# Kernel tuning notes

Measured on AMD Instinct MI355X. Metric: run time of the kernel, lower is better.

Reference implementation:

```python
import jax, jax.numpy as jnp
import numpy as np

N = 50000      # nodes
E = 800000     # edges
DIN = 500      # input feature dim
H = 128        # hidden dim
C = 40         # num classes
B = 10000      # batch_size (labeled nodes)
L = 9          # n_layers
K = 5          # topk neighbors
ALPHA = 0.5
THETA = 1.0
ETA = 0.5


def setup_inputs() -> dict:
    key = jax.random.key(0)
    ks = jax.random.split(key, 10)
    x = jax.random.normal(ks[0], (N, DIN), jnp.float32)
    edge_index = jax.random.randint(ks[1], (2, E), 0, N, dtype=jnp.int32)
    edge_weight = jax.random.uniform(ks[2], (E,), jnp.float32)
    y = jax.random.randint(ks[3], (B,), 0, C, dtype=jnp.int32)
    W1 = jax.random.normal(ks[4], (DIN, H), jnp.float32) * 0.05
    b1 = jnp.zeros((H,), jnp.float32)
    conv_w1 = jax.random.normal(ks[5], (L, H, H), jnp.float32) * 0.05
    conv_w2 = jax.random.normal(ks[6], (L, H, H), jnp.float32) * 0.05
    W2 = jax.random.normal(ks[7], (H, C), jnp.float32) * 0.05
    b2 = jnp.zeros((C,), jnp.float32)
    return dict(x=x, edge_index=edge_index, edge_weight=edge_weight, y=y,
                batch_size=B, W1=W1, b1=b1, conv_w1=conv_w1, conv_w2=conv_w2,
                W2=W2, b2=b2)


def _spmm(edge_index, edge_weight, h):
    # out[row] += w * h[col]  (sparse adj_t @ h)
    row, col = edge_index[0], edge_index[1]
    msg = h[col] * edge_weight[:, None]           # [E, H]
    return jax.ops.segment_sum(msg, row, num_segments=N)


def reference(x, edge_index, edge_weight, y, batch_size, W1, b1, conv_w1, conv_w2, W2, b2):
    # eval mode: dropout is identity, no diagonal mask in label fusion
    h = jax.nn.relu(x @ W1 + b1)                  # [N, H]
    x0 = h
    for l in range(L):
        beta = float(np.log(THETA / (l + 1) + 1.0))
        p = _spmm(edge_index, edge_weight, h) * (1.0 - ALPHA)   # propagated, scaled
        xr = ALPHA * x0                                          # initial residual
        out = ((1.0 - beta) * p + beta * (p @ conv_w1[l])
               + (1.0 - beta) * xr + beta * (xr @ conv_w2[l]))
        h = jax.nn.relu(h + out)
    emb = h[:batch_size]                          # [B, H]
    logits = h @ W2 + b2
    p_lc = jax.nn.log_softmax(logits[:batch_size], axis=1)       # [B, C]
    # kNN label fusion: cosine similarity, topk, exp-weighted one-hot sum
    an = emb / jnp.clip(jnp.linalg.norm(emb, axis=1, keepdims=True), 1e-8)
    sim = an @ an.T                               # [B, B]
    vals, idx = jax.lax.top_k(sim, K)             # [B, K]
    w = jnp.exp(jax.lax.stop_gradient(vals))      # topk computed under no_grad
    onehot = jax.nn.one_hot(y, C, dtype=jnp.float32)             # [B, C]
    fused = jnp.einsum('bk,bkc->bc', w, onehot[idx])             # [B, C]
    p_sim = jax.nn.log_softmax(fused, axis=1)
    final = ETA * p_lc + (1.0 - ETA) * p_sim
    return final, emb
```

## Files before the change

### kernel.cpp

```cpp
#include <hip/hip_runtime.h>
#include <hip/hip_bf16.h>
#include <math.h>

#define Nn  50000
#define NR  50048
#define En  800000
#define DIN 500
#define Hd  128
#define Cc  40
#define Bb  10000
#define Ll  9
#define KT  5

typedef short bf16x8 __attribute__((ext_vector_type(8)));
typedef unsigned short u16x8 __attribute__((ext_vector_type(8)));
typedef float f32x4 __attribute__((ext_vector_type(4)));

__device__ inline float bf2f(unsigned short u) {
  union { unsigned int i; float f; } c; c.i = (unsigned int)u << 16; return c.f;
}
__device__ inline unsigned short f2bf(float f) {
  __hip_bfloat16 b = __float2bfloat16(f);
  return *(unsigned short*)&b;
}

__global__ __launch_bounds__(256) void k_pack_w1(const float* __restrict__ W1,
                                                 unsigned short* __restrict__ W1p) {
  const int id = blockIdx.x * 256 + threadIdx.x;
  if (id >= 65536) return;
  const int j = id & 7, col = (id >> 3) & 127, qk = id >> 10;
  const int k = (qk >> 2) * 32 + (qk & 3) * 8 + j;
  W1p[id] = f2bf((k < DIN) ? W1[(size_t)k * Hd + col] : 0.f);
}

__global__ __launch_bounds__(256) void k_pack_wc(const float* __restrict__ cw1,
    const float* __restrict__ cw2, unsigned short* __restrict__ Wcp) {
  const int id = blockIdx.x * 256 + threadIdx.x;
  if (id >= 294912) return;
  const int j = id & 7, col = (id >> 3) & 127, qk = (id >> 10) & 31, l = id >> 15;
  const int k = (qk >> 2) * 32 + (qk & 3) * 8 + j;
  float v;
  if (k < 128) v = cw1[((size_t)l * 128 + k) * 128 + col];
  else         v = 0.5f * cw2[((size_t)l * 128 + (k - 128)) * 128 + col];
  Wcp[id] = f2bf(v);
}

__global__ __launch_bounds__(256) void k_in(const float* __restrict__ x,
    const unsigned short* __restrict__ W1p, const float* __restrict__ b1,
    unsigned short* __restrict__ hb, unsigned short* __restrict__ x0b) {
  const int tid = threadIdx.x;
  const int wv = tid >> 6, lane = tid & 63;
  const int lrow = lane & 15, quad = lane >> 4;
  const int row0 = blockIdx.x * 64;
  const int ar = row0 + wv * 16 + lrow;
  f32x4 acc[8];
#pragma unroll
  for (int t = 0; t < 8; ++t) acc[t] = (f32x4){0.f, 0.f, 0.f, 0.f};

  for (int kk = 0; kk < 16; ++kk) {
    const int kbase = kk * 32 + quad * 8;
    float av[8];
    if (ar < Nn) {
      if (kk < 15) {
        const float4 p0 = *(const float4*)(x + (size_t)ar * DIN + kbase);
        const float4 p1 = *(const float4*)(x + (size_t)ar * DIN + kbase + 4);
        av[0] = p0.x; av[1] = p0.y; av[2] = p0.z; av[3] = p0.w;
        av[4] = p1.x; av[5] = p1.y; av[6] = p1.z; av[7] = p1.w;
      } else {
#pragma unroll
        for (int j = 0; j < 8; ++j)
          av[j] = (kbase + j < DIN) ? x[(size_t)ar * DIN + kbase + j] : 0.f;
      }
    } else {
#pragma unroll
      for (int j = 0; j < 8; ++j) av[j] = 0.f;
    }
    bf16x8 af;
#pragma unroll
    for (int j = 0; j < 8; ++j) af[j] = (short)f2bf(av[j]);
#pragma unroll
    for (int nt = 0; nt < 8; ++nt) {
      const bf16x8 bf = *(const bf16x8*)(W1p + ((size_t)(kk * 4 + quad) * 128 + nt * 16 + lrow) * 8);
      acc[nt] = __builtin_amdgcn_mfma_f32_16x16x32_bf16(af, bf, acc[nt], 0, 0, 0);
    }
  }

  __shared__ float sacc[64 * 132];
#pragma unroll
  for (int nt = 0; nt < 8; ++nt)
#pragma unroll
    for (int i = 0; i < 4; ++i)
      sacc[(wv * 16 + quad * 4 + i) * 132 + nt * 16 + lrow] = acc[nt][i];
  __syncthreads();

  const int row = tid >> 2, cs = (tid & 3) * 32;
  const int gr = row0 + row;
  if (gr < Nn) {
#pragma unroll
    for (int g = 0; g < 4; ++g) {
      const int c0 = cs + g * 8;
      float v[8];
#pragma unroll
      for (int j = 0; j < 8; ++j)
        v[j] = fmaxf(sacc[row * 132 + c0 + j] + b1[c0 + j], 0.f);
      u16x8 ob;
#pragma unroll
      for (int j = 0; j < 8; ++j) ob[j] = f2bf(v[j]);
      *(u16x8*)(hb + (size_t)gr * Hd + c0) = ob;
      *(u16x8*)(x0b + (size_t)gr * Hd + c0) = ob;
    }
  }
}

__global__ void k_hist(const int* __restrict__ rows, int* __restrict__ counts) {
  int e = blockIdx.x * 256 + threadIdx.x;
  if (e < En) atomicAdd(&counts[rows[e]], 1);
}

__global__ __launch_bounds__(1024) void k_scan(const int* __restrict__ counts,
                                               int* __restrict__ ptr) {
  __shared__ int buf[1024];
  __shared__ int s_base;
  const int tid = threadIdx.x;
  if (tid == 0) { s_base = 0; ptr[0] = 0; }
  __syncthreads();
  for (int start = 0; start < Nn; start += 1024) {
    int i = start + tid;
    int v = (i < Nn) ? counts[i] : 0;
    buf[tid] = v;
    __syncthreads();
    for (int off = 1; off < 1024; off <<= 1) {
      int t = (tid >= off) ? buf[tid - off] : 0;
      __syncthreads();
      buf[tid] += t;
      __syncthreads();
    }
    if (i < Nn) ptr[i + 1] = s_base + buf[tid];
    __syncthreads();
    if (tid == 0) s_base += buf[1023];
    __syncthreads();
  }
}

__global__ void k_scatter(const int* __restrict__ rows, const int* __restrict__ cols,
                          const float* __restrict__ w, const int* __restrict__ ptr,
                          int* __restrict__ fill, int* __restrict__ csr_col,
                          float* __restrict__ csr_w) {
  int e = blockIdx.x * 256 + threadIdx.x;
  if (e >= En) return;
  int r = rows[e];
  int pos = atomicAdd(&fill[r], 1);
  int d = ptr[r] + pos;
  csr_col[d] = cols[e];
  csr_w[d] = w[e];
}

__global__ __launch_bounds__(256) void k_spmm(const int* __restrict__ ptr,
    const int* __restrict__ csr_col, const float* __restrict__ csr_w,
    const unsigned short* __restrict__ hb, unsigned short* __restrict__ pb) {
  const int wave = (blockIdx.x * 256 + threadIdx.x) >> 6;
  const int lane = threadIdx.x & 63;
  const int g = lane >> 4;
  const int fl = lane & 15;
  if (wave >= Nn) return;
  const int s = ptr[wave], e_end = ptr[wave + 1];
  float acc[8];
#pragma unroll
  for (int j = 0; j < 8; ++j) acc[j] = 0.f;

  auto acc8 = [&](uint4 v, float w) {
    union { unsigned int i; float f; } t;
    t.i = v.x << 16;         acc[0] += w * t.f;
    t.i = v.x & 0xFFFF0000u; acc[1] += w * t.f;
    t.i = v.y << 16;         acc[2] += w * t.f;
    t.i = v.y & 0xFFFF0000u; acc[3] += w * t.f;
    t.i = v.z << 16;         acc[4] += w * t.f;
    t.i = v.z & 0xFFFF0000u; acc[5] += w * t.f;
    t.i = v.w << 16;         acc[6] += w * t.f;
    t.i = v.w & 0xFFFF0000u; acc[7] += w * t.f;
  };

  int e = s + g;
  for (; e + 12 < e_end; e += 16) {
    const int c0 = csr_col[e];
    const int c1 = csr_col[e + 4];
    const int c2 = csr_col[e + 8];
    const int c3 = csr_col[e + 12];
    const float w0 = csr_w[e];
    const float w1 = csr_w[e + 4];
    const float w2 = csr_w[e + 8];
    const float w3 = csr_w[e + 12];
    const uint4 v0 = *(const uint4*)(hb + (size_t)c0 * Hd + fl * 8);
    const uint4 v1 = *(const uint4*)(hb + (size_t)c1 * Hd + fl * 8);
    const uint4 v2 = *(const uint4*)(hb + (size_t)c2 * Hd + fl * 8);
    const uint4 v3 = *(const uint4*)(hb + (size_t)c3 * Hd + fl * 8);
    acc8(v0, w0); acc8(v1, w1); acc8(v2, w2); acc8(v3, w3);
  }
  for (; e + 4 < e_end; e += 8) {
    const int c0 = csr_col[e];
    const int c1 = csr_col[e + 4];
    const float w0 = csr_w[e];
    const float w1 = csr_w[e + 4];
    const uint4 v0 = *(const uint4*)(hb + (size_t)c0 * Hd + fl * 8);
    const uint4 v1 = *(const uint4*)(hb + (size_t)c1 * Hd + fl * 8);
    acc8(v0, w0); acc8(v1, w1);
  }
  if (e < e_end) {
    const int c = csr_col[e];
    const float w = csr_w[e];
    const uint4 v = *(const uint4*)(hb + (size_t)c * Hd + fl * 8);
    acc8(v, w);
  }
#pragma unroll
  for (int j = 0; j < 8; ++j) acc[j] += __shfl_xor(acc[j], 16);
#pragma unroll
  for (int j = 0; j < 8; ++j) acc[j] += __shfl_xor(acc[j], 32);
  if (g == 0) {
    uint4 o;
    o.x = (unsigned int)f2bf(0.5f * acc[0]) | ((unsigned int)f2bf(0.5f * acc[1]) << 16);
    o.y = (unsigned int)f2bf(0.5f * acc[2]) | ((unsigned int)f2bf(0.5f * acc[3]) << 16);
    o.z = (unsigned int)f2bf(0.5f * acc[4]) | ((unsigned int)f2bf(0.5f * acc[5]) << 16);
    o.w = (unsigned int)f2bf(0.5f * acc[6]) | ((unsigned int)f2bf(0.5f * acc[7]) << 16);
    *(uint4*)(pb + (size_t)wave * Hd + fl * 8) = o;
  }
}

__global__ __launch_bounds__(256) void k_layer(const unsigned short* __restrict__ pb,
    const unsigned short* __restrict__ x0b, const unsigned short* __restrict__ Wcp,
    unsigned short* __restrict__ hb, float beta) {
  const int tid = threadIdx.x;
  const int wv = tid >> 6, lane = tid & 63;
  const int lrow = lane & 15, quad = lane >> 4;
  const int row0 = blockIdx.x * 64;
  const int ar = row0 + wv * 16 + lrow;
  f32x4 acc[8];
#pragma unroll
  for (int t = 0; t < 8; ++t) acc[t] = (f32x4){0.f, 0.f, 0.f, 0.f};

#pragma unroll
  for (int kk = 0; kk < 8; ++kk) {
    const unsigned short* src = (kk < 4) ? pb : x0b;
    const int ko = (kk & 3) * 32 + quad * 8;
    const bf16x8 af = *(const bf16x8*)(src + (size_t)ar * Hd + ko);
#pragma unroll
    for (int nt = 0; nt < 8; ++nt) {
      const bf16x8 bf = *(const bf16x8*)(Wcp + ((size_t)(kk * 4 + quad) * 128 + nt * 16 + lrow) * 8);
      acc[nt] = __builtin_amdgcn_mfma_f32_16x16x32_bf16(af, bf, acc[nt], 0, 0, 0);
    }
  }

  __shared__ float sacc[64 * 132];
#pragma unroll
  for (int nt = 0; nt < 8; ++nt)
#pragma unroll
    for (int i = 0; i < 4; ++i)
      sacc[(wv * 16 + quad * 4 + i) * 132 + nt * 16 + lrow] = acc[nt][i];
  __syncthreads();

  const int row = tid >> 2, cs = (tid & 3) * 32;
  const int gr = row0 + row;
  if (gr < Nn) {
    const float om = 1.f - beta;
#pragma unroll
    for (int g = 0; g < 4; ++g) {
      const int c0 = cs + g * 8;
      const u16x8 pv = *(const u16x8*)(pb + (size_t)gr * Hd + c0);
      const u16x8 xv = *(const u16x8*)(x0b + (size_t)gr * Hd + c0);
      const u16x8 hv = *(const u16x8*)(hb + (size_t)gr * Hd + c0);
      float nv[8];
#pragma unroll
      for (int j = 0; j < 8; ++j) {
        const float gemm = sacc[row * 132 + c0 + j];
        const float pj = bf2f(pv[j]);
        const float xj = bf2f(xv[j]);
        const float outv = om * (pj + 0.5f * xj) + beta * gemm;
        nv[j] = fmaxf(bf2f(hv[j]) + outv, 0.f);
      }
      u16x8 ob;
#pragma unroll
      for (int j = 0; j < 8; ++j) ob[j] = f2bf(nv[j]);
      *(u16x8*)(hb + (size_t)gr * Hd + c0) = ob;
    }
  }
}

__global__ __launch_bounds__(256) void k_head(const unsigned short* __restrict__ hb,
    const float* __restrict__ W2, const float* __restrict__ b2,
    unsigned short* __restrict__ anb, float* __restrict__ p_lc,
    float* __restrict__ out_emb) {
  const int wid = (blockIdx.x * 256 + threadIdx.x) >> 6;
  const int lane = threadIdx.x & 63;
  if (wid >= Bb) return;
  const unsigned short* hr = hb + (size_t)wid * Hd;
  const float v0 = bf2f(hr[lane]), v1 = bf2f(hr[lane + 64]);
  out_emb[wid * Hd + lane] = v0;
  out_emb[wid * Hd + lane + 64] = v1;
  float ss = v0 * v0 + v1 * v1;
#pragma unroll
  for (int off = 32; off > 0; off >>= 1) ss += __shfl_xor(ss, off);
  const float inv = 1.f / fmaxf(sqrtf(ss), 1e-8f);
  anb[wid * Hd + lane] = f2bf(v0 * inv);
  anb[wid * Hd + lane + 64] = f2bf(v1 * inv);
  float l = 0.f;
  if (lane < Cc) {
    for (int k = 0; k < Hd; ++k) l += bf2f(hr[k]) * W2[k * Cc + lane];
    l += b2[lane];
  }
  float lm = (lane < Cc) ? l : -3.0e38f;
#pragma unroll
  for (int off = 32; off > 0; off >>= 1) lm = fmaxf(lm, __shfl_xor(lm, off));
  float ex = (lane < Cc) ? expf(l - lm) : 0.f;
#pragma unroll
  for (int off = 32; off > 0; off >>= 1) ex += __shfl_xor(ex, off);
  const float lse = logf(ex);
  if (lane < Cc) p_lc[wid * Cc + lane] = l - lm - lse;
}

#define CH_N  4
#define CH_SZ 2500
#define SB_LD 136
__global__ __launch_bounds__(256) void k_simtopk(const unsigned short* __restrict__ anb,
    float* __restrict__ cval, int* __restrict__ cidx) {
  __shared__ __align__(16) char smem[40960];
  unsigned short* sb = (unsigned short*)smem;
  const int rt = blockIdx.x / CH_N;
  const int chunk = blockIdx.x % CH_N;
  const int row0 = rt * 64;
  const int cbeg = chunk * CH_SZ;
  const int cend = cbeg + CH_SZ;
  const int tid = threadIdx.x;
  const int wv = tid >> 6;
  const int lane = tid & 63;
  const int lrow = lane & 15;
  const int quad = lane >> 4;

  union Frag { uint4 u4; bf16x8 v; };
  bf16x8 afr[4];
  const int ar = row0 + wv * 16 + lrow;
#pragma unroll
  for (int kq = 0; kq < 4; ++kq) {
    Frag f;
    f.u4 = make_uint4(0u, 0u, 0u, 0u);
    if (ar < Bb) f.u4 = *(const uint4*)(anb + (size_t)ar * Hd + kq * 32 + quad * 8);
    afr[kq] = f.v;
  }

  float bv[4][KT];
  int bi[4][KT];
#pragma unroll
  for (int r = 0; r < 4; ++r)
#pragma unroll
    for (int t = 0; t < KT; ++t) { bv[r][t] = -3.0e38f; bi[r][t] = 0x7fffffff; }

  const int ntile = (CH_SZ + 63) / 64;
  for (int t = 0; t < ntile; ++t) {
    const int c0 = cbeg + t * 64;
    __syncthreads();
    for (int i = tid; i < 1024; i += 256) {
      const int r = i >> 4, ch = i & 15;
      const int gc = c0 + r;
      uint4 v = make_uint4(0u, 0u, 0u, 0u);
      if (gc < cend) v = *(const uint4*)(anb + (size_t)gc * Hd + ch * 8);
      *(uint4*)&sb[r * SB_LD + ch * 8] = v;
    }
    __syncthreads();
#pragma unroll
    for (int sub = 0; sub < 4; ++sub) {
      f32x4 acc = {0.f, 0.f, 0.f, 0.f};
      const int scol = sub * 16 + lrow;
#pragma unroll
      for (int kq = 0; kq < 4; ++kq) {
        bf16x8 bfr = *(const bf16x8*)&sb[scol * SB_LD + kq * 32 + quad * 8];
        acc = __builtin_amdgcn_mfma_f32_16x16x32_bf16(afr[kq], bfr, acc, 0, 0, 0);
      }
      const int gc = c0 + scol;
      const bool ok = gc < cend;
#pragma unroll
      for (int i = 0; i < 4; ++i) {
        const float v = ok ? acc[i] : -3.0e38f;
        if (v > bv[i][KT - 1]) {
          float tv = v; int ti = gc;
#pragma unroll
          for (int s = 0; s < KT; ++s) {
            if (tv > bv[i][s]) {
              float ov = bv[i][s]; int oi = bi[i][s];
              bv[i][s] = tv; bi[i][s] = ti; tv = ov; ti = oi;
            }
          }
        }
      }
    }
  }

  __syncthreads();
  float* mv = (float*)smem;
  int* mi = (int*)(smem + 20480);
#pragma unroll
  for (int i = 0; i < 4; ++i) {
    const int row = wv * 16 + quad * 4 + i;
#pragma unroll
    for (int t = 0; t < KT; ++t) {
      mv[row * 80 + lrow * KT + t] = bv[i][t];
      mi[row * 80 + lrow * KT + t] = bi[i][t];
    }
  }
  __syncthreads();
  if (tid < 64) {
    const int gr = row0 + tid;
    if (gr < Bb) {
      float tv5[KT]; int ti5[KT];
#pragma unroll
      for (int t = 0; t < KT; ++t) { tv5[t] = -3.0e38f; ti5[t] = 0x7fffffff; }
      for (int m = 0; m < 80; ++m) {
        float v = mv[tid * 80 + m]; int id = mi[tid * 80 + m];
        if (v > tv5[KT - 1] || (v == tv5[KT - 1] && id < ti5[KT - 1])) {
#pragma unroll
          for (int s = 0; s < KT; ++s) {
            if (v > tv5[s] || (v == tv5[s] && id < ti5[s])) {
              float ov = tv5[s]; int oi = ti5[s];
              tv5[s] = v; ti5[s] = id; v = ov; id = oi;
            }
          }
        }
      }
#pragma unroll
      for (int t = 0; t < KT; ++t) {
        cval[gr * (CH_N * KT) + chunk * KT + t] = tv5[t];
        cidx[gr * (CH_N * KT) + chunk * KT + t] = ti5[t];
      }
    }
  }
}

__global__ __launch_bounds__(256) void k_final(const float* __restrict__ cval,
    const int* __restrict__ cidx, const int* __restrict__ y,
    const float* __restrict__ p_lc, float* __restrict__ out_final) {
  const int b = blockIdx.x * 256 + threadIdx.x;
  if (b >= Bb) return;
  float tv5[KT]; int ti5[KT];
#pragma unroll
  for (int t = 0; t < KT; ++t) { tv5[t] = -3.0e38f; ti5[t] = 0x7fffffff; }
#pragma unroll
  for (int m = 0; m < CH_N * KT; ++m) {
    float v = cval[b * (CH_N * KT) + m]; int id = cidx[b * (CH_N * KT) + m];
    if (v > tv5[KT - 1] || (v == tv5[KT - 1] && id < ti5[KT - 1])) {
#pragma unroll
      for (int t = 0; t < KT; ++t) {
        if (v > tv5[t] || (v == tv5[t] && id < ti5[t])) {
          float ov = tv5[t]; int oi = ti5[t];
          tv5[t] = v; ti5[t] = id; v = ov; id = oi;
        }
      }
    }
  }
  float w[KT]; int cls[KT];
#pragma unroll
  for (int t = 0; t < KT; ++t) { w[t] = expf(tv5[t]); cls[t] = y[ti5[t]]; }
  float m = -3.0e38f;
  for (int c = 0; c < Cc; ++c) {
    float f = 0.f;
#pragma unroll
    for (int t = 0; t < KT; ++t) f += (cls[t] == c) ? w[t] : 0.f;
    m = fmaxf(m, f);
  }
  float s = 0.f;
  for (int c = 0; c < Cc; ++c) {
    float f = 0.f;
#pragma unroll
    for (int t = 0; t < KT; ++t) f += (cls[t] == c) ? w[t] : 0.f;
    s += expf(f - m);
  }
  const float lse = logf(s);
  for (int c = 0; c < Cc; ++c) {
    float f = 0.f;
#pragma unroll
    for (int t = 0; t < KT; ++t) f += (cls[t] == c) ? w[t] : 0.f;
    out_final[b * Cc + c] = 0.5f * p_lc[b * Cc + c] + 0.5f * (f - m - lse);
  }
}

extern "C" void kernel_launch(void* const* d_in, const int* in_sizes, int n_in,
                              void* d_out, int out_size, void* d_ws, size_t ws_size,
                              hipStream_t stream) {
  const float* x  = (const float*)d_in[0];
  const int* erow = (const int*)d_in[1];
  const int* ecol = erow + En;
  const float* ew = (const float*)d_in[2];
  const int* y    = (const int*)d_in[3];
  const float* W1 = (const float*)d_in[5];
  const float* b1 = (const float*)d_in[6];
  const float* cw1 = (const float*)d_in[7];
  const float* cw2 = (const float*)d_in[8];
  const float* W2 = (const float*)d_in[9];
  const float* b2 = (const float*)d_in[10];
  float* out = (float*)d_out;

  float* ws = (float*)d_ws;
  size_t off = 0;
  float* plc = ws + off; off += (size_t)Bb * Cc;
  float* cval = ws + off; off += (size_t)Bb * (CH_N * KT);
  int* cidx  = (int*)(ws + off); off += (size_t)Bb * (CH_N * KT);
  int* counts = (int*)(ws + off); off += Nn;
  int* fill   = (int*)(ws + off); off += Nn;
  int* rptr   = (int*)(ws + off); off += Nn + 4;
  int* ccol   = (int*)(ws + off); off += En;
  float* cwt  = ws + off; off += En;
  unsigned short* anb = (unsigned short*)(ws + off); off += (size_t)Bb * Hd / 2;
  unsigned short* hb  = (unsigned short*)(ws + off); off += (size_t)NR * Hd / 2;
  unsigned short* x0b = (unsigned short*)(ws + off); off += (size_t)NR * Hd / 2;
  unsigned short* pb  = (unsigned short*)(ws + off); off += (size_t)NR * Hd / 2;
  unsigned short* W1p = (unsigned short*)(ws + off); off += 65536 / 2;
  unsigned short* Wcp = (unsigned short*)(ws + off); off += 294912 / 2;

  k_pack_w1<<<256, 256, 0, stream>>>(W1, W1p);
  k_pack_wc<<<1152, 256, 0, stream>>>(cw1, cw2, Wcp);
  k_in<<<NR / 64, 256, 0, stream>>>(x, W1p, b1, hb, x0b);
  hipMemsetAsync(counts, 0, (size_t)2 * Nn * sizeof(int), stream);
  k_hist<<<(En + 255) / 256, 256, 0, stream>>>(erow, counts);
  k_scan<<<1, 1024, 0, stream>>>(counts, rptr);
  k_scatter<<<(En + 255) / 256, 256, 0, stream>>>(erow, ecol, ew, rptr, fill, ccol, cwt);
  for (int l = 0; l < Ll; ++l) {
    const float beta = logf(1.0f / (float)(l + 1) + 1.0f);
    k_spmm<<<(Nn * 64 + 255) / 256, 256, 0, stream>>>(rptr, ccol, cwt, hb, pb);
    k_layer<<<NR / 64, 256, 0, stream>>>(pb, x0b, Wcp + (size_t)l * 32768, hb, beta);
  }
  k_head<<<(Bb * 64) / 256, 256, 0, stream>>>(hb, W2, b2, anb, plc, out + (size_t)Bb * Cc);
  k_simtopk<<<((Bb + 63) / 64) * CH_N, 256, 0, stream>>>(anb, cval, cidx);
  k_final<<<(Bb + 255) / 256, 256, 0, stream>>>(cval, cidx, y, plc, out);
}
```

Baseline: 1.069 ms.

## Parallelize CSR scan, split similarity top-k into more chunks, add early-reject threshold

The single-block prefix scan over node counts is replaced by a multi-block kernel. Each block reduces all preceding counts to get its base offset, then runs a local 256-wide scan. The similarity top-k kernel now splits columns into 8 chunks instead of 4, giving more blocks and more candidates to merge. It also skips per-row insertion when no value in a 4-row group beats the smallest current top-k threshold. The multi-block scan does redundant prefix reads that grow with block index, and the final merge step now handles twice as many candidates.

```diff
diff --git a/kernel.cpp b/kernel.cpp
--- a/kernel.cpp
+++ b/kernel.cpp
@@ -117,29 +117,37 @@
   if (e < En) atomicAdd(&counts[rows[e]], 1);
 }
 
-__global__ __launch_bounds__(1024) void k_scan(const int* __restrict__ counts,
-                                               int* __restrict__ ptr) {
-  __shared__ int buf[1024];
-  __shared__ int s_base;
-  const int tid = threadIdx.x;
-  if (tid == 0) { s_base = 0; ptr[0] = 0; }
-  __syncthreads();
-  for (int start = 0; start < Nn; start += 1024) {
-    int i = start + tid;
-    int v = (i < Nn) ? counts[i] : 0;
-    buf[tid] = v;
+__global__ __launch_bounds__(256) void k_scan2(const int* __restrict__ counts,
+                                               int* __restrict__ rptr) {
+  __shared__ int sdata[256];
+  const int b = blockIdx.x, tid = threadIdx.x;
+  const int npre = b << 8;
+  int s0 = 0, s1 = 0, s2 = 0, s3 = 0;
+  int i = tid;
+  for (; i + 768 < npre; i += 1024) {
+    s0 += counts[i]; s1 += counts[i + 256]; s2 += counts[i + 512]; s3 += counts[i + 768];
+  }
+  for (; i < npre; i += 256) s0 += counts[i];
+  sdata[tid] = s0 + s1 + s2 + s3;
+  __syncthreads();
+  for (int off = 128; off > 0; off >>= 1) {
+    if (tid < off) sdata[tid] += sdata[tid + off];
     __syncthreads();
-    for (int off = 1; off < 1024; off <<= 1) {
-      int t = (tid >= off) ? buf[tid - off] : 0;
-      __syncthreads();
-      buf[tid] += t;
-      __syncthreads();
-    }
-    if (i < Nn) ptr[i + 1] = s_base + buf[tid];
+  }
+  const int base = sdata[0];
+  __syncthreads();
+  const int gi = npre + tid;
+  int v = (gi < Nn) ? counts[gi] : 0;
+  sdata[tid] = v;
+  __syncthreads();
+  for (int off = 1; off < 256; off <<= 1) {
+    int t = (tid >= off) ? sdata[tid - off] : 0;
     __syncthreads();
-    if (tid == 0) s_base += buf[1023];
+    sdata[tid] += t;
     __syncthreads();
   }
+  if (gi < Nn) rptr[gi + 1] = base + sdata[tid];
+  if (b == 0 && tid == 0) rptr[0] = 0;
 }
 
 __global__ void k_scatter(const int* __restrict__ rows, const int* __restrict__ cols,
@@ -316,8 +324,8 @@
   if (lane < Cc) p_lc[wid * Cc + lane] = l - lm - lse;
 }
 
-#define CH_N  4
-#define CH_SZ 2500
+#define CH_N  8
+#define CH_SZ 1250
 #define SB_LD 136
 __global__ __launch_bounds__(256) void k_simtopk(const unsigned short* __restrict__ anb,
     float* __restrict__ cval, int* __restrict__ cidx) {
@@ -351,6 +359,7 @@
   for (int r = 0; r < 4; ++r)
 #pragma unroll
     for (int t = 0; t < KT; ++t) { bv[r][t] = -3.0e38f; bi[r][t] = 0x7fffffff; }
+  float minthr = -3.0e38f;
 
   const int ntile = (CH_SZ + 63) / 64;
   for (int t = 0; t < ntile; ++t) {
@@ -375,19 +384,27 @@
       }
       const int gc = c0 + scol;
       const bool ok = gc < cend;
-#pragma unroll
-      for (int i = 0; i < 4; ++i) {
-        const float v = ok ? acc[i] : -3.0e38f;
-        if (v > bv[i][KT - 1]) {
-          float tv = v; int ti = gc;
-#pragma unroll
-          for (int s = 0; s < KT; ++s) {
-            if (tv > bv[i][s]) {
-              float ov = bv[i][s]; int oi = bi[i][s];
-              bv[i][s] = tv; bi[i][s] = ti; tv = ov; ti = oi;
+      float vv[4];
+#pragma unroll
+      for (int i = 0; i < 4; ++i) vv[i] = ok ? acc[i] : -3.0e38f;
+      const float mx = fmaxf(fmaxf(vv[0], vv[1]), fmaxf(vv[2], vv[3]));
+      if (mx > minthr) {
+#pragma unroll
+        for (int i = 0; i < 4; ++i) {
+          const float v = vv[i];
+          if (v > bv[i][KT - 1]) {
+            float tv = v; int ti = gc;
+#pragma unroll
+            for (int s = 0; s < KT; ++s) {
+              if (tv > bv[i][s]) {
+                float ov = bv[i][s]; int oi = bi[i][s];
+                bv[i][s] = tv; bi[i][s] = ti; tv = ov; ti = oi;
+              }
             }
           }
         }
+        minthr = fminf(fminf(bv[0][KT - 1], bv[1][KT - 1]),
+                       fminf(bv[2][KT - 1], bv[3][KT - 1]));
       }
     }
   }
@@ -517,7 +534,7 @@
   k_in<<<NR / 64, 256, 0, stream>>>(x, W1p, b1, hb, x0b);
   hipMemsetAsync(counts, 0, (size_t)2 * Nn * sizeof(int), stream);
   k_hist<<<(En + 255) / 256, 256, 0, stream>>>(erow, counts);
-  k_scan<<<1, 1024, 0, stream>>>(counts, rptr);
+  k_scan2<<<(Nn + 255) / 256, 256, 0, stream>>>(counts, rptr);
   k_scatter<<<(En + 255) / 256, 256, 0, stream>>>(erow, ecol, ew, rptr, fill, ccol, cwt);
   for (int l = 0; l < Ll; ++l) {
     const float beta = logf(1.0f / (float)(l + 1) + 1.0f);
```

Result: faster. 1.012 ms (-5.3%).
